# Optimization experiments

Hardware: AMD Instinct MI355X
Metric: run time of the kernel (lower is better)

Reference implementation:

```python
import jax, jax.numpy as jnp
import numpy as np

SD = 4          # spixel_downsize
EPS = 1e-5      # BatchNorm eps
SLOPE = 0.01    # nn.LeakyReLU() default negative_slope


def deconv3d(x, w, stride, pad):
    # w is in torch ConvTranspose3d layout: (in_ch, out_ch, kd, kh, kw).
    # Transposed conv == conv with lhs_dilation=stride, flipped kernel,
    # padding (k-1-p) per spatial dim.
    kd, kh, kw = w.shape[2], w.shape[3], w.shape[4]
    wc = jnp.transpose(jnp.flip(w, axis=(2, 3, 4)), (1, 0, 2, 3, 4))  # OIDHW
    pads = [(kd - 1 - pad[0],) * 2, (kh - 1 - pad[1],) * 2, (kw - 1 - pad[2],) * 2]
    return jax.lax.conv_general_dilated(
        x, wc, window_strides=(1, 1, 1), padding=pads,
        lhs_dilation=(stride, stride, stride),
        dimension_numbers=('NCDHW', 'OIDHW', 'NCDHW'))


def bn_lrelu(x, g, b, relu=True):
    # inference BatchNorm3d with running_mean=0, running_var=1 (fresh BN)
    scale = (g / jnp.sqrt(1.0 + EPS)).reshape(1, -1, 1, 1, 1)
    y = x * scale + b.reshape(1, -1, 1, 1, 1)
    return jax.nn.leaky_relu(y, SLOPE) if relu else y


def _sl(s):
    # shift s in {+1, 0, -1} -> (agg slice, cost slice) along one spatial dim
    if s == 1:
        return slice(SD, None), slice(None, -SD)
    if s == 0:
        return slice(None), slice(None)
    return slice(None, -SD), slice(SD, None)


def setup_inputs() -> dict:
    key = jax.random.key(0)
    ks = jax.random.split(key, 8)
    b, d, h, w = 1, 24, 64, 128
    f32 = jnp.float32
    cv1 = jax.random.normal(ks[0], (b, 32, d, h, w), f32)                 # cv[-1]
    cv0 = jax.random.normal(ks[1], (b, 16, 2 * d, 2 * h, 2 * w), f32)     # cv[-2]
    sp = jax.random.uniform(ks[2], (b, 9, 4 * h, 4 * w), f32)             # superpixel probs
    w0a = jax.random.normal(ks[3], (32, 32, 3, 1, 1), f32) * 0.05
    w0b = jax.random.normal(ks[4], (32, 16, 4, 2, 2), f32) * 0.05
    w1a = jax.random.normal(ks[5], (32, 16, 3, 1, 1), f32) * 0.05
    w1b = jax.random.normal(ks[6], (16, 1, 4, 2, 2), f32) * 0.05
    g0, g1, g2, g3 = (jnp.ones((c,), f32) for c in (32, 16, 16, 1))
    b0, b1, b2, b3 = (jnp.zeros((c,), f32) for c in (32, 16, 16, 1))
    return dict(cv1=cv1, cv0=cv0, sp=sp, w0a=w0a, w0b=w0b, w1a=w1a, w1b=w1b,
                g0=g0, g1=g1, g2=g2, g3=g3, b0=b0, b1=b1, b2=b2, b3=b3)


def reference(cv1, cv0, sp, w0a, w0b, w1a, w1b, g0, g1, g2, g3, b0, b1, b2, b3):
    # conv[0]: BasicConv(32->32, k(3,1,1), s1, p(1,0,0)) + BasicConv(32->16, k(4,2,2), s2, p(1,0,0))
    x = bn_lrelu(deconv3d(cv1, w0a, 1, (1, 0, 0)), g0, b0)
    x = bn_lrelu(deconv3d(x, w0b, 2, (1, 0, 0)), g1, b1)
    x = jnp.concatenate((x, cv0), axis=1)
    # conv[1] (sp==2 branch): 32->16 then 16->out_dim, bn=relu=bnrelu=True
    x = bn_lrelu(deconv3d(x, w1a, 1, (1, 0, 0)), g2, b2)
    cost = bn_lrelu(deconv3d(x, w1b, 2, (1, 0, 0)), g3, b3)  # (b, 1, 4d, 4h, 4w)

    sp5 = sp[:, None]  # (b, 1, 9, H, W)
    agg = jnp.zeros_like(cost)
    k = 0
    for hy in (1, 0, -1):        # 9 fixed superpixel-neighbor shifts
        ah, ch = _sl(hy)
        for wx in (1, 0, -1):
            aw, cw = _sl(wx)
            wgt = sp5[:, :, k, ah, aw][:, :, None]  # (b,1,1,H',W')
            agg = agg.at[:, :, :, ah, aw].add(cost[:, :, :, ch, cw] * wgt)
            k += 1
    return agg
```

## Files before the change

### kernel.cpp

```cpp
#include <hip/hip_runtime.h>
#include <hip/hip_bf16.h>

typedef __hip_bfloat16 bf16;

constexpr int cD0 = 24,  cH0 = 64,  cW0 = 128;
constexpr int cD1 = 48,  cH1 = 128, cW1 = 256;
constexpr int cD2 = 96,  cH2 = 256, cW2 = 512;
constexpr size_t PL0 = (size_t)cD0 * cH0 * cW0;
constexpr size_t PL1 = (size_t)cD1 * cH1 * cW1;
constexpr size_t PL2 = (size_t)cD2 * cH2 * cW2;

__device__ __forceinline__ float b2f(bf16 v) { return __bfloat162float(v); }
__device__ __forceinline__ bf16  f2b(float v) { return __float2bfloat16(v); }
__device__ __forceinline__ float lrelu(float v) { return v >= 0.f ? v : 0.01f * v; }
__device__ __forceinline__ float us2f(ushort u) { return __uint_as_float(((uint)u) << 16); }
__device__ __forceinline__ ushort f2us(float v) { return __bfloat16_as_ushort(f2b(v)); }

__global__ __launch_bounds__(256) void kA(const float* __restrict__ cv1,
                                          const float* __restrict__ w0a,
                                          const float* __restrict__ g0,
                                          const float* __restrict__ b0,
                                          bf16* __restrict__ x1) {
    __shared__ float lw[3][32][32];
    __shared__ float lsc[32], lbi[32];
    const int tid = threadIdx.x;
    for (int i = tid; i < 32 * 32 * 3; i += 256) {
        int ci = i / 96, r = i - ci * 96, co = r / 3, u = r - co * 3;
        lw[u][ci][co] = w0a[i];
    }
    if (tid < 32) {
        lsc[tid] = g0[tid] * (1.0f / sqrtf(1.0f + 1e-5f));
        lbi[tid] = b0[tid];
    }
    __syncthreads();

    const int pos = blockIdx.x * 256 + tid;
    const int x = pos & (cW0 - 1);
    const int y = (pos >> 7) & (cH0 - 1);
    const int z = pos >> 13;

    float acc[32];
    #pragma unroll
    for (int co = 0; co < 32; ++co) acc[co] = 0.f;

    #pragma unroll
    for (int u = 0; u < 3; ++u) {
        const int zi = z + 1 - u;
        if (zi < 0 || zi >= cD0) continue;
        const float* src = cv1 + (size_t)(zi * cH0 + y) * cW0 + x;
        for (int ci = 0; ci < 32; ++ci) {
            const float v = src[ci * PL0];
            const float4* wp = (const float4*)&lw[u][ci][0];
            #pragma unroll
            for (int q = 0; q < 8; ++q) {
                float4 wv = wp[q];
                acc[4*q+0] += v * wv.x; acc[4*q+1] += v * wv.y;
                acc[4*q+2] += v * wv.z; acc[4*q+3] += v * wv.w;
            }
        }
    }
    #pragma unroll
    for (int co = 0; co < 32; ++co)
        x1[co * PL0 + (size_t)(z * cH0 + y) * cW0 + x] =
            f2b(lrelu(acc[co] * lsc[co] + lbi[co]));
}

__global__ __launch_bounds__(256) void kB(const bf16* __restrict__ x1,
                                          const float* __restrict__ w0b,
                                          const float* __restrict__ g1,
                                          const float* __restrict__ b1,
                                          bf16* __restrict__ x2) {
    __shared__ float lw[4][2][32][2][16];
    __shared__ float lsc[16], lbi[16];
    const int tid = threadIdx.x;
    for (int i = tid; i < 8192; i += 256) {
        int ci = i >> 8, co = (i >> 4) & 15, kd = (i >> 2) & 3, kh = (i >> 1) & 1, kw = i & 1;
        lw[kd][kh][ci][kw][co] = w0b[i];
    }
    if (tid < 16) {
        lsc[tid] = g1[tid] * (1.0f / sqrtf(1.0f + 1e-5f));
        lbi[tid] = b1[tid];
    }
    __syncthreads();

    const int t    = blockIdx.x * 256 + tid;
    const int lane = t & 63;
    const int wv_  = (t >> 6) & 3;
    const int b_   = t >> 8;
    const int oh = b_ & 127;
    const int od = (b_ >> 7) * 4 + wv_;
    const int ih = oh >> 1, kh = oh & 1;
    const int kw = lane & 1;
    const int p  = (od + 1) & 1;
    const int iwb = lane >> 1;

    float acc[4][16];
    #pragma unroll
    for (int k = 0; k < 4; ++k)
        #pragma unroll
        for (int co = 0; co < 16; ++co) acc[k][co] = 0.f;

    #pragma unroll
    for (int j = 0; j < 2; ++j) {
        const int kd = p + 2 * j;
        const int id = (od + 1 - kd) >> 1;
        if (id < 0 || id >= cD0) continue;
        const bf16* src = x1 + (size_t)(id * cH0 + ih) * cW0 + iwb;
        for (int ci = 0; ci < 32; ++ci) {
            const float v0 = b2f(src[ci * PL0 +  0]);
            const float v1 = b2f(src[ci * PL0 + 32]);
            const float v2 = b2f(src[ci * PL0 + 64]);
            const float v3 = b2f(src[ci * PL0 + 96]);
            const float4* wp = (const float4*)&lw[kd][kh][ci][kw][0];
            #pragma unroll
            for (int q = 0; q < 4; ++q) {
                float4 wv = wp[q];
                acc[0][4*q+0] += v0 * wv.x; acc[0][4*q+1] += v0 * wv.y;
                acc[0][4*q+2] += v0 * wv.z; acc[0][4*q+3] += v0 * wv.w;
                acc[1][4*q+0] += v1 * wv.x; acc[1][4*q+1] += v1 * wv.y;
                acc[1][4*q+2] += v1 * wv.z; acc[1][4*q+3] += v1 * wv.w;
                acc[2][4*q+0] += v2 * wv.x; acc[2][4*q+1] += v2 * wv.y;
                acc[2][4*q+2] += v2 * wv.z; acc[2][4*q+3] += v2 * wv.w;
                acc[3][4*q+0] += v3 * wv.x; acc[3][4*q+1] += v3 * wv.y;
                acc[3][4*q+2] += v3 * wv.z; acc[3][4*q+3] += v3 * wv.w;
            }
        }
    }
    const size_t obase = (size_t)(od * cH1 + oh) * cW1 + lane;
    #pragma unroll
    for (int k = 0; k < 4; ++k)
        #pragma unroll
        for (int co = 0; co < 16; ++co)
            x2[co * PL1 + obase + 64 * k] =
                f2b(lrelu(acc[k][co] * lsc[co] + lbi[co]));
}

__global__ __launch_bounds__(256) void kD(const bf16* __restrict__ x2,
                                          const float* __restrict__ cv0,
                                          const float* __restrict__ w1a,
                                          const float* __restrict__ g2,
                                          const float* __restrict__ b2v,
                                          bf16* __restrict__ x3) {
    __shared__ float lw[3][32][16];
    __shared__ float lsc[16], lbi[16];
    const int tid = threadIdx.x;
    for (int i = tid; i < 1536; i += 256) {
        int ci = i / 48, r = i - ci * 48, co = r / 3, u = r - co * 3;
        lw[u][ci][co] = w1a[i];
    }
    if (tid < 16) {
        lsc[tid] = g2[tid] * (1.0f / sqrtf(1.0f + 1e-5f));
        lbi[tid] = b2v[tid];
    }
    __syncthreads();

    const int bid = blockIdx.x;
    const int b_  = (bid & 7) * 384 + (bid >> 3);
    const int zq = b_ % 12;
    const int yh = b_ / 12;
    const int h  = yh & 1;
    const int y  = yh >> 1;
    const int lane = tid & 63;
    const int wv_  = tid >> 6;
    const int z  = zq * 4 + wv_;
    const int x0 = h * 128 + 2 * lane;

    float acc[2][16];
    #pragma unroll
    for (int k = 0; k < 2; ++k)
        #pragma unroll
        for (int co = 0; co < 16; ++co) acc[k][co] = 0.f;

    #pragma unroll
    for (int u = 0; u < 3; ++u) {
        const int zi = z + 1 - u;
        if (zi < 0 || zi >= cD1) continue;
        const size_t base = (size_t)(zi * cH1 + y) * cW1 + x0;
        #pragma unroll 4
        for (int ci = 0; ci < 16; ++ci) {
            const uint pk = *(const uint*)(x2 + ci * PL1 + base);
            const float v0 = us2f((ushort)(pk & 0xffffu));
            const float v1 = us2f((ushort)(pk >> 16));
            const float4* wp = (const float4*)&lw[u][ci][0];
            #pragma unroll
            for (int q = 0; q < 4; ++q) {
                float4 wv = wp[q];
                acc[0][4*q+0] += v0 * wv.x; acc[0][4*q+1] += v0 * wv.y;
                acc[0][4*q+2] += v0 * wv.z; acc[0][4*q+3] += v0 * wv.w;
                acc[1][4*q+0] += v1 * wv.x; acc[1][4*q+1] += v1 * wv.y;
                acc[1][4*q+2] += v1 * wv.z; acc[1][4*q+3] += v1 * wv.w;
            }
        }
        #pragma unroll 4
        for (int ci = 0; ci < 16; ++ci) {
            const float2 fv = *(const float2*)(cv0 + ci * PL1 + base);
            const float v0 = fv.x, v1 = fv.y;
            const float4* wp = (const float4*)&lw[u][16 + ci][0];
            #pragma unroll
            for (int q = 0; q < 4; ++q) {
                float4 wv = wp[q];
                acc[0][4*q+0] += v0 * wv.x; acc[0][4*q+1] += v0 * wv.y;
                acc[0][4*q+2] += v0 * wv.z; acc[0][4*q+3] += v0 * wv.w;
                acc[1][4*q+0] += v1 * wv.x; acc[1][4*q+1] += v1 * wv.y;
                acc[1][4*q+2] += v1 * wv.z; acc[1][4*q+3] += v1 * wv.w;
            }
        }
    }
    const size_t obase = (size_t)(z * cH1 + y) * cW1 + x0;
    #pragma unroll
    for (int co = 0; co < 16; ++co) {
        union { uint u32; ushort s[2]; } pk;
        pk.s[0] = f2us(lrelu(acc[0][co] * lsc[co] + lbi[co]));
        pk.s[1] = f2us(lrelu(acc[1][co] * lsc[co] + lbi[co]));
        *(uint*)(x3 + co * PL1 + obase) = pk.u32;
    }
}

__global__ __launch_bounds__(256) void kE(const bf16* __restrict__ x3,
                                          const float* __restrict__ w1b,
                                          const float* __restrict__ g3,
                                          const float* __restrict__ b3v,
                                          bf16* __restrict__ cost) {
    __shared__ float lw[256];
    const int tid = threadIdx.x;
    lw[tid] = w1b[tid];
    __syncthreads();

    const int t    = blockIdx.x * 256 + tid;
    const int lane = t & 63;
    const int wv_  = (t >> 6) & 3;
    const int b_   = t >> 8;
    const int iwp = lane + 64 * (b_ & 1);
    const int ih  = (b_ >> 1) & 127;
    const int od  = (b_ >> 8) * 4 + wv_;
    const int p   = (od + 1) & 1;
    const int iw0 = 2 * iwp;

    float a[2][2][2] = {};
    #pragma unroll
    for (int j = 0; j < 2; ++j) {
        const int kd = p + 2 * j;
        const int id = (od + 1 - kd) >> 1;
        if (id < 0 || id >= cD1) continue;
        const size_t base = (size_t)(id * cH1 + ih) * cW1 + iw0;
        #pragma unroll
        for (int ci = 0; ci < 16; ++ci) {
            const uint pk = *(const uint*)(x3 + ci * PL1 + base);
            const float v0 = us2f((ushort)(pk & 0xffffu));
            const float v1 = us2f((ushort)(pk >> 16));
            const float* w = &lw[ci * 16 + kd * 4];
            a[0][0][0] += v0 * w[0]; a[0][0][1] += v0 * w[1];
            a[0][1][0] += v0 * w[2]; a[0][1][1] += v0 * w[3];
            a[1][0][0] += v1 * w[0]; a[1][0][1] += v1 * w[1];
            a[1][1][0] += v1 * w[2]; a[1][1][1] += v1 * w[3];
        }
    }
    const float sc = g3[0] * (1.0f / sqrtf(1.0f + 1e-5f));
    const float bi = b3v[0];
    const size_t ob = (size_t)(od * cH2 + 2 * ih) * cW2 + 4 * iwp;
    ushort4 s;
    s.x = f2us(lrelu(a[0][0][0] * sc + bi));
    s.y = f2us(lrelu(a[0][0][1] * sc + bi));
    s.z = f2us(lrelu(a[1][0][0] * sc + bi));
    s.w = f2us(lrelu(a[1][0][1] * sc + bi));
    *(ushort4*)(cost + ob) = s;
    s.x = f2us(lrelu(a[0][1][0] * sc + bi));
    s.y = f2us(lrelu(a[0][1][1] * sc + bi));
    s.z = f2us(lrelu(a[1][1][0] * sc + bi));
    s.w = f2us(lrelu(a[1][1][1] * sc + bi));
    *(ushort4*)(cost + ob + cW2) = s;
}

__global__ __launch_bounds__(256) void kF(const bf16* __restrict__ cost,
                                          const float* __restrict__ sp,
                                          float* __restrict__ out) {
    const int t    = blockIdx.x * 256 + threadIdx.x;
    const int lane = t & 63;
    const int rowq = t >> 6;
    const int x0 = 4 * (lane + 64 * (rowq & 1));
    const int y  = (rowq >> 1) & 255;
    const int d0 = (rowq >> 9) * 4;
    const size_t plane = (size_t)cH2 * cW2;

    float4 wq[9];
    int cyc[3], cxc[3];
    #pragma unroll
    for (int r = 0; r < 3; ++r) {
        const int cy = y - 4 * (1 - r);
        const bool vy = (cy >= 0) && (cy < cH2);
        cyc[r] = vy ? cy : 0;
        #pragma unroll
        for (int c = 0; c < 3; ++c) {
            const int cx = x0 - 4 * (1 - c);
            const bool vx = (cx >= 0) && (cx < cW2);
            if (r == 0) cxc[c] = vx ? cx : 0;
            if (vy && vx)
                wq[r*3+c] = *(const float4*)(sp + (size_t)(r*3+c) * plane + (size_t)y * cW2 + x0);
            else
                wq[r*3+c] = make_float4(0.f, 0.f, 0.f, 0.f);
        }
    }
    #pragma unroll
    for (int dd = 0; dd < 4; ++dd) {
        const int d = d0 + dd;
        const bf16* cp = cost + (size_t)d * plane;
        float ax = 0.f, ay = 0.f, az = 0.f, aw = 0.f;
        #pragma unroll
        for (int r = 0; r < 3; ++r) {
            const bf16* rp = cp + (size_t)cyc[r] * cW2;
            #pragma unroll
            for (int c = 0; c < 3; ++c) {
                const ushort4 u = *(const ushort4*)(rp + cxc[c]);
                const float4 w = wq[r*3+c];
                ax += w.x * us2f(u.x); ay += w.y * us2f(u.y);
                az += w.z * us2f(u.z); aw += w.w * us2f(u.w);
            }
        }
        float4 o; o.x = ax; o.y = ay; o.z = az; o.w = aw;
        *(float4*)(out + (size_t)d * plane + (size_t)y * cW2 + x0) = o;
    }
}

extern "C" void kernel_launch(void* const* d_in, const int* in_sizes, int n_in,
                              void* d_out, int out_size, void* d_ws, size_t ws_size,
                              hipStream_t stream) {
    const float* cv1 = (const float*)d_in[0];
    const float* cv0 = (const float*)d_in[1];
    const float* sp  = (const float*)d_in[2];
    const float* w0a = (const float*)d_in[3];
    const float* w0b = (const float*)d_in[4];
    const float* w1a = (const float*)d_in[5];
    const float* w1b = (const float*)d_in[6];
    const float* g0  = (const float*)d_in[7];
    const float* g1  = (const float*)d_in[8];
    const float* g2  = (const float*)d_in[9];
    const float* g3  = (const float*)d_in[10];
    const float* b0  = (const float*)d_in[11];
    const float* b1  = (const float*)d_in[12];
    const float* b2  = (const float*)d_in[13];
    const float* b3  = (const float*)d_in[14];

    char* ws = (char*)d_ws;
    bf16* x1   = (bf16*)(ws);
    bf16* x2   = (bf16*)(ws + 12582912);
    bf16* x3   = (bf16*)(ws + 62914560);
    bf16* cost = (bf16*)(ws);

    kA<<<768,  256, 0, stream>>>(cv1, w0a, g0, b0, x1);
    kB<<<1536, 256, 0, stream>>>(x1, w0b, g1, b1, x2);
    kD<<<3072, 256, 0, stream>>>(x2, cv0, w1a, g2, b2, x3);
    kE<<<6144, 256, 0, stream>>>(x3, w1b, g3, b3, cost);
    kF<<<3072, 256, 0, stream>>>(cost, sp, (float*)d_out);
}
```

Measured before the change: 378.0 us.

## Batch channel loads into registers and vectorize kB input/output access

In kA, kD and kE the per-channel global loads are hoisted into register arrays before the FMA loops, so all loads are in flight at once instead of interleaved with compute. kB is remapped so each lane reads two adjacent bf16 inputs with one 32-bit load and writes four adjacent outputs with one ushort4 store, using both kw weight sets per input. The intent is more memory-level parallelism and wider, more coalesced accesses, at the cost of higher register pressure that may reduce occupancy.

```diff
diff --git a/kernel.cpp b/kernel.cpp
--- a/kernel.cpp
+++ b/kernel.cpp
@@ -48,14 +48,17 @@
         const int zi = z + 1 - u;
         if (zi < 0 || zi >= cD0) continue;
         const float* src = cv1 + (size_t)(zi * cH0 + y) * cW0 + x;
+        float v[32];
+        #pragma unroll
+        for (int ci = 0; ci < 32; ++ci) v[ci] = src[ci * PL0];
+        #pragma unroll
         for (int ci = 0; ci < 32; ++ci) {
-            const float v = src[ci * PL0];
             const float4* wp = (const float4*)&lw[u][ci][0];
             #pragma unroll
             for (int q = 0; q < 8; ++q) {
                 float4 wv = wp[q];
-                acc[4*q+0] += v * wv.x; acc[4*q+1] += v * wv.y;
-                acc[4*q+2] += v * wv.z; acc[4*q+3] += v * wv.w;
+                acc[4*q+0] += v[ci] * wv.x; acc[4*q+1] += v[ci] * wv.y;
+                acc[4*q+2] += v[ci] * wv.z; acc[4*q+3] += v[ci] * wv.w;
             }
         }
     }
@@ -90,9 +93,8 @@
     const int oh = b_ & 127;
     const int od = (b_ >> 7) * 4 + wv_;
     const int ih = oh >> 1, kh = oh & 1;
-    const int kw = lane & 1;
     const int p  = (od + 1) & 1;
-    const int iwb = lane >> 1;
+    const int iw0 = 2 * lane;
 
     float acc[4][16];
     #pragma unroll
@@ -105,34 +107,41 @@
         const int kd = p + 2 * j;
         const int id = (od + 1 - kd) >> 1;
         if (id < 0 || id >= cD0) continue;
-        const bf16* src = x1 + (size_t)(id * cH0 + ih) * cW0 + iwb;
+        const bf16* src = x1 + (size_t)(id * cH0 + ih) * cW0 + iw0;
+        uint px[32];
+        #pragma unroll
+        for (int ci = 0; ci < 32; ++ci)
+            px[ci] = *(const uint*)(src + ci * PL0);
+        #pragma unroll
         for (int ci = 0; ci < 32; ++ci) {
-            const float v0 = b2f(src[ci * PL0 +  0]);
-            const float v1 = b2f(src[ci * PL0 + 32]);
-            const float v2 = b2f(src[ci * PL0 + 64]);
-            const float v3 = b2f(src[ci * PL0 + 96]);
-            const float4* wp = (const float4*)&lw[kd][kh][ci][kw][0];
+            const float v0 = us2f((ushort)(px[ci] & 0xffffu));
+            const float v1 = us2f((ushort)(px[ci] >> 16));
+            const float4* wp0 = (const float4*)&lw[kd][kh][ci][0][0];
+            const float4* wp1 = (const float4*)&lw[kd][kh][ci][1][0];
             #pragma unroll
             for (int q = 0; q < 4; ++q) {
-                float4 wv = wp[q];
-                acc[0][4*q+0] += v0 * wv.x; acc[0][4*q+1] += v0 * wv.y;
-                acc[0][4*q+2] += v0 * wv.z; acc[0][4*q+3] += v0 * wv.w;
-                acc[1][4*q+0] += v1 * wv.x; acc[1][4*q+1] += v1 * wv.y;
-                acc[1][4*q+2] += v1 * wv.z; acc[1][4*q+3] += v1 * wv.w;
-                acc[2][4*q+0] += v2 * wv.x; acc[2][4*q+1] += v2 * wv.y;
-                acc[2][4*q+2] += v2 * wv.z; acc[2][4*q+3] += v2 * wv.w;
-                acc[3][4*q+0] += v3 * wv.x; acc[3][4*q+1] += v3 * wv.y;
-                acc[3][4*q+2] += v3 * wv.z; acc[3][4*q+3] += v3 * wv.w;
-            }
-        }
-    }
-    const size_t obase = (size_t)(od * cH1 + oh) * cW1 + lane;
-    #pragma unroll
-    for (int k = 0; k < 4; ++k)
-        #pragma unroll
-        for (int co = 0; co < 16; ++co)
-            x2[co * PL1 + obase + 64 * k] =
-                f2b(lrelu(acc[k][co] * lsc[co] + lbi[co]));
+                float4 w0 = wp0[q], w1 = wp1[q];
+                acc[0][4*q+0] += v0 * w0.x; acc[0][4*q+1] += v0 * w0.y;
+                acc[0][4*q+2] += v0 * w0.z; acc[0][4*q+3] += v0 * w0.w;
+                acc[1][4*q+0] += v0 * w1.x; acc[1][4*q+1] += v0 * w1.y;
+                acc[1][4*q+2] += v0 * w1.z; acc[1][4*q+3] += v0 * w1.w;
+                acc[2][4*q+0] += v1 * w0.x; acc[2][4*q+1] += v1 * w0.y;
+                acc[2][4*q+2] += v1 * w0.z; acc[2][4*q+3] += v1 * w0.w;
+                acc[3][4*q+0] += v1 * w1.x; acc[3][4*q+1] += v1 * w1.y;
+                acc[3][4*q+2] += v1 * w1.z; acc[3][4*q+3] += v1 * w1.w;
+            }
+        }
+    }
+    const size_t obase = (size_t)(od * cH1 + oh) * cW1 + 4 * lane;
+    #pragma unroll
+    for (int co = 0; co < 16; ++co) {
+        ushort4 s;
+        s.x = f2us(lrelu(acc[0][co] * lsc[co] + lbi[co]));
+        s.y = f2us(lrelu(acc[1][co] * lsc[co] + lbi[co]));
+        s.z = f2us(lrelu(acc[2][co] * lsc[co] + lbi[co]));
+        s.w = f2us(lrelu(acc[3][co] * lsc[co] + lbi[co]));
+        *(ushort4*)(x2 + co * PL1 + obase) = s;
+    }
 }
 
 __global__ __launch_bounds__(256) void kD(const bf16* __restrict__ x2,
@@ -176,11 +185,18 @@
         const int zi = z + 1 - u;
         if (zi < 0 || zi >= cD1) continue;
         const size_t base = (size_t)(zi * cH1 + y) * cW1 + x0;
-        #pragma unroll 4
+        uint   px[16];
+        float2 pc[16];
+        #pragma unroll
+        for (int ci = 0; ci < 16; ++ci)
+            px[ci] = *(const uint*)(x2 + ci * PL1 + base);
+        #pragma unroll
+        for (int ci = 0; ci < 16; ++ci)
+            pc[ci] = *(const float2*)(cv0 + ci * PL1 + base);
+        #pragma unroll
         for (int ci = 0; ci < 16; ++ci) {
-            const uint pk = *(const uint*)(x2 + ci * PL1 + base);
-            const float v0 = us2f((ushort)(pk & 0xffffu));
-            const float v1 = us2f((ushort)(pk >> 16));
+            const float v0 = us2f((ushort)(px[ci] & 0xffffu));
+            const float v1 = us2f((ushort)(px[ci] >> 16));
             const float4* wp = (const float4*)&lw[u][ci][0];
             #pragma unroll
             for (int q = 0; q < 4; ++q) {
@@ -191,10 +207,9 @@
                 acc[1][4*q+2] += v1 * wv.z; acc[1][4*q+3] += v1 * wv.w;
             }
         }
-        #pragma unroll 4
+        #pragma unroll
         for (int ci = 0; ci < 16; ++ci) {
-            const float2 fv = *(const float2*)(cv0 + ci * PL1 + base);
-            const float v0 = fv.x, v1 = fv.y;
+            const float v0 = pc[ci].x, v1 = pc[ci].y;
             const float4* wp = (const float4*)&lw[u][16 + ci][0];
             #pragma unroll
             for (int q = 0; q < 4; ++q) {
@@ -243,11 +258,14 @@
         const int id = (od + 1 - kd) >> 1;
         if (id < 0 || id >= cD1) continue;
         const size_t base = (size_t)(id * cH1 + ih) * cW1 + iw0;
+        uint px[16];
+        #pragma unroll
+        for (int ci = 0; ci < 16; ++ci)
+            px[ci] = *(const uint*)(x3 + ci * PL1 + base);
         #pragma unroll
         for (int ci = 0; ci < 16; ++ci) {
-            const uint pk = *(const uint*)(x3 + ci * PL1 + base);
-            const float v0 = us2f((ushort)(pk & 0xffffu));
-            const float v1 = us2f((ushort)(pk >> 16));
+            const float v0 = us2f((ushort)(px[ci] & 0xffffu));
+            const float v1 = us2f((ushort)(px[ci] >> 16));
             const float* w = &lw[ci * 16 + kd * 4];
             a[0][0][0] += v0 * w[0]; a[0][0][1] += v0 * w[1];
             a[0][1][0] += v0 * w[2]; a[0][1][1] += v0 * w[3];
```

Result: slower. 411.1 us (+8.8%).
